# Kernel tuning notes

Measured on AMD Instinct MI355X. Metric: run time of the kernel, lower is better.

## Reference

```python
import jax, jax.numpy as jnp
import numpy as np

B, C, H, W = 32, 256, 64, 64
N_HEAD, LDIM = 4, 64
HW = H * W
SCALE = float(np.sqrt(LDIM))
EPS = 1e-5


def setup_inputs() -> dict:
    key = jax.random.key(0)
    ks = jax.random.split(key, 8)
    inp = {
        "x": jax.random.normal(ks[0], (B, C, H, W), dtype=jnp.float32),
        "x1": jax.random.normal(ks[1], (B, C, H, W), dtype=jnp.float32),
        # linear weights stored as [in, out] (transposed torch layout)
        "Wq": jax.random.normal(ks[2], (HW, N_HEAD * LDIM), dtype=jnp.float32) * 0.02,
        "Wk": jax.random.normal(ks[3], (HW, N_HEAD * LDIM), dtype=jnp.float32) * 0.02,
        "Wv": jax.random.normal(ks[4], (HW, N_HEAD * LDIM), dtype=jnp.float32) * 0.02,
        "Wfc": jax.random.normal(ks[5], (N_HEAD * LDIM, HW), dtype=jnp.float32) * 0.02,
        "gamma": jnp.ones((C,), dtype=jnp.float32),
        "beta": jnp.zeros((C,), dtype=jnp.float32),
    }
    return inp


def reference(x, x1, Wq, Wk, Wv, Wfc, gamma, beta):
    b, c, h, w = x.shape
    xf = x.reshape(b, c, h * w)    # [b, c, hw]
    x1f = x1.reshape(b, c, h * w)
    # projections: [b, c, hw] @ [hw, n*d] -> [b, c, n*d]
    q = (xf @ Wq).reshape(b, c, N_HEAD, LDIM).transpose(0, 2, 1, 3)   # [b, n, c, d]
    k = (x1f @ Wk).reshape(b, c, N_HEAD, LDIM).transpose(0, 2, 1, 3)
    v = (x1f @ Wv).reshape(b, c, N_HEAD, LDIM).transpose(0, 2, 1, 3)
    # scaled dot-product attention over the c 'channel-token' axis
    attn = jnp.einsum('bncd,bnmd->bncm', q / SCALE, k)  # [b, n, c, c]
    attn = jax.nn.softmax(attn, axis=-1)
    out = jnp.einsum('bncm,bnmd->bncd', attn, v)        # [b, n, c, d]
    out = out.transpose(0, 2, 1, 3).reshape(b, c, N_HEAD * LDIM)
    out = (out @ Wfc).reshape(b, c, h, w)
    # BatchNorm2d (training-mode batch statistics, biased variance)
    mean = out.mean(axis=(0, 2, 3), keepdims=True)
    var = out.var(axis=(0, 2, 3), keepdims=True)
    out = (out - mean) * jax.lax.rsqrt(var + EPS)
    out = out * gamma[None, :, None, None] + beta[None, :, None, None]
    return out
```

## Files before the change

### kernel.cpp

```cpp
#include <hip/hip_runtime.h>
#include <hip/hip_bf16.h>

#define Bsz 32
#define Csz 256
#define HWsz 4096
#define NDsz 256
#define Msz 8192

typedef __bf16 bf16x8 __attribute__((ext_vector_type(8)));
typedef float  f32x4  __attribute__((ext_vector_type(4)));
typedef short  s16x4  __attribute__((ext_vector_type(4)));
typedef short  s16x8  __attribute__((ext_vector_type(8)));

__device__ __forceinline__ unsigned short f2bf(float f){
  unsigned u = __float_as_uint(f);
  u += 0x7FFFu + ((u >> 16) & 1u);
  return (unsigned short)(u >> 16);
}

__device__ __forceinline__ f32x4 mfma16(bf16x8 a, bf16x8 b, f32x4 c){
  return __builtin_amdgcn_mfma_f32_16x16x32_bf16(a, b, c, 0, 0, 0);
}

__global__ void k_prep(const float* __restrict__ Wq, const float* __restrict__ Wk,
                       const float* __restrict__ Wv, const float* __restrict__ Wfc,
                       unsigned short* __restrict__ Wt, unsigned short* __restrict__ Wfct){
  __shared__ float t[32][33];
  int z = blockIdx.z;
  int bx = blockIdx.x, by = blockIdx.y;
  const float* src; unsigned short* dst; int R, Ct;
  if (z < 3) {
    src = (z == 0) ? Wq : (z == 1 ? Wk : Wv);
    dst = Wt + (size_t)z * Csz * HWsz;  R = HWsz; Ct = NDsz;
  } else {
    int tidx = bx * 8 + by; bx = tidx & 7; by = tidx >> 3;
    src = Wfc; dst = Wfct; R = NDsz; Ct = HWsz;
  }
  int tx = threadIdx.x, ty = threadIdx.y;
  int i0 = bx * 32, j0 = by * 32;
  #pragma unroll
  for (int r = 0; r < 4; r++)
    t[ty + 8*r][tx] = src[(size_t)(i0 + ty + 8*r) * Ct + j0 + tx];
  __syncthreads();
  #pragma unroll
  for (int r = 0; r < 4; r++)
    dst[(size_t)(j0 + ty + 8*r) * R + i0 + tx] = f2bf(t[tx][ty + 8*r]);
}

__global__ __launch_bounds__(256, 3) void k_proj(const float* __restrict__ X,
    const float* __restrict__ X1, const unsigned short* __restrict__ Wt,
    unsigned short* __restrict__ QKV){
  const int wgid = blockIdx.x;
  const int xcd = wgid & 7, q = wgid >> 3;
  const int rtHi = q / 6, m = q - rtHi * 6;
  const int rt = rtHi * 8 + xcd;
  const int which = m >> 1, ct = m & 1;

  const float* A = (which == 0) ? X : X1;
  const unsigned short* Bt = Wt + (size_t)which * NDsz * HWsz;
  unsigned short* Cp = QKV + (size_t)which * Msz * NDsz;

  __shared__ unsigned short As[64][72];
  __shared__ unsigned short Bs[128][72];

  const int tid = threadIdx.x;
  const int lane = tid & 63, w = tid >> 6;
  const int l15 = lane & 15, l4 = lane >> 4;
  const int wm = w >> 1, wn = w & 1;

  const int arow = tid >> 2, acol = (tid & 3) * 16;
  const float* agp = A + (size_t)(rt*64 + arow) * HWsz + acol;
  const int brow = tid >> 1, bcol = (tid & 1) * 32;
  const unsigned short* bgp = Bt + (size_t)(ct*128 + brow) * HWsz + bcol;

  f32x4 acc[2][4] = {};
  float4 ar[4];
  s16x8 br[4];

#define LOADA(kt) { _Pragma("unroll") for (int i = 0; i < 4; i++) \
    ar[i] = *(const float4*)(agp + (size_t)(kt)*64 + i*4); }
#define LOADB(kt) { _Pragma("unroll") for (int p = 0; p < 4; p++) \
    br[p] = *(const s16x8*)(bgp + (size_t)(kt)*64 + p*8); }
#define WRITEAB { _Pragma("unroll") for (int i = 0; i < 4; i++){ s16x4 cv; \
      cv[0]=(short)f2bf(ar[i].x); cv[1]=(short)f2bf(ar[i].y); \
      cv[2]=(short)f2bf(ar[i].z); cv[3]=(short)f2bf(ar[i].w); \
      *(s16x4*)&As[arow][acol + i*4] = cv; } \
    _Pragma("unroll") for (int p = 0; p < 4; p++) *(s16x8*)&Bs[brow][bcol + p*8] = br[p]; }

  LOADA(0); LOADB(0);
  WRITEAB;
  __syncthreads();

  const int NK = HWsz / 64;
  for (int kt = 1; kt <= NK; kt++){
    const bool more = (kt < NK);
    if (more){ LOADA(kt); LOADB(kt); }
    #pragma unroll
    for (int kk = 0; kk < 2; kk++){
      bf16x8 a[2], b[4];
      #pragma unroll
      for (int fm = 0; fm < 2; fm++) a[fm] = *(const bf16x8*)&As[wm*32 + fm*16 + l15][kk*32 + l4*8];
      #pragma unroll
      for (int fn = 0; fn < 4; fn++) b[fn] = *(const bf16x8*)&Bs[wn*64 + fn*16 + l15][kk*32 + l4*8];
      #pragma unroll
      for (int fm = 0; fm < 2; fm++)
        #pragma unroll
        for (int fn = 0; fn < 4; fn++)
          acc[fm][fn] = mfma16(a[fm], b[fn], acc[fm][fn]);
    }
    if (more){
      __syncthreads();
      WRITEAB;
      __syncthreads();
    }
  }
#undef LOADA
#undef LOADB
#undef WRITEAB
  #pragma unroll
  for (int fm = 0; fm < 2; fm++)
    #pragma unroll
    for (int fn = 0; fn < 4; fn++)
      #pragma unroll
      for (int r = 0; r < 4; r++)
        Cp[(size_t)(rt*64 + wm*32 + fm*16 + l4*4 + r) * NDsz
           + ct*128 + wn*64 + fn*16 + l15] = f2bf(acc[fm][fn][r]);
}

__global__ __launch_bounds__(256) void k_attn(const unsigned short* __restrict__ Q,
    const unsigned short* __restrict__ K, const unsigned short* __restrict__ V,
    unsigned short* __restrict__ O){
  const int b = blockIdx.x >> 3, n = (blockIdx.x >> 1) & 3, half = blockIdx.x & 1;
  __shared__ unsigned short VT[64][264];
  __shared__ unsigned short PL[4][32][72];

  const int tid = threadIdx.x;
  const int lane = tid & 63, w = tid >> 6;
  const int l15 = lane & 15, l4 = lane >> 4;

  {
    const unsigned short* vp = V + (size_t)(b*256 + tid) * NDsz + n*64;
    #pragma unroll
    for (int j = 0; j < 8; j++){
      s16x8 vv = *(const s16x8*)(vp + j*8);
      #pragma unroll
      for (int e = 0; e < 8; e++) VT[j*8 + e][tid] = (unsigned short)vv[e];
    }
  }

  const int qbase = b*256 + half*128 + w*32;
  bf16x8 qf[2][2];
  #pragma unroll
  for (int fm = 0; fm < 2; fm++)
    #pragma unroll
    for (int ks = 0; ks < 2; ks++)
      qf[fm][ks] = *(const bf16x8*)(Q + (size_t)(qbase + fm*16 + l15) * NDsz
                                      + n*64 + ks*32 + l4*8);

  f32x4 oacc[2][4] = {};
  float rs[2][4] = {};
  __syncthreads();

  for (int ch = 0; ch < 4; ch++){
    f32x4 sacc[2][4] = {};
    #pragma unroll
    for (int ks = 0; ks < 2; ks++){
      bf16x8 kf[4];
      #pragma unroll
      for (int fn = 0; fn < 4; fn++)
        kf[fn] = *(const bf16x8*)(K + (size_t)(b*256 + ch*64 + fn*16 + l15) * NDsz
                                    + n*64 + ks*32 + l4*8);
      #pragma unroll
      for (int fm = 0; fm < 2; fm++)
        #pragma unroll
        for (int fn = 0; fn < 4; fn++)
          sacc[fm][fn] = mfma16(qf[fm][ks], kf[fn], sacc[fm][fn]);
    }
    #pragma unroll
    for (int fm = 0; fm < 2; fm++)
      #pragma unroll
      for (int fn = 0; fn < 4; fn++)
        #pragma unroll
        for (int r = 0; r < 4; r++){
          float e = __expf(sacc[fm][fn][r] * 0.125f);
          rs[fm][r] += e;
          PL[w][fm*16 + l4*4 + r][fn*16 + l15] = f2bf(e);
        }
    #pragma unroll
    for (int ks = 0; ks < 2; ks++){
      bf16x8 pa[2], vb[4];
      #pragma unroll
      for (int fm = 0; fm < 2; fm++)
        pa[fm] = *(const bf16x8*)&PL[w][fm*16 + l15][ks*32 + l4*8];
      #pragma unroll
      for (int fn = 0; fn < 4; fn++)
        vb[fn] = *(const bf16x8*)&VT[fn*16 + l15][ch*64 + ks*32 + l4*8];
      #pragma unroll
      for (int fm = 0; fm < 2; fm++)
        #pragma unroll
        for (int fn = 0; fn < 4; fn++)
          oacc[fm][fn] = mfma16(pa[fm], vb[fn], oacc[fm][fn]);
    }
  }
  #pragma unroll
  for (int fm = 0; fm < 2; fm++)
    #pragma unroll
    for (int r = 0; r < 4; r++){
      float s = rs[fm][r];
      s += __shfl_xor(s, 1, 16); s += __shfl_xor(s, 2, 16);
      s += __shfl_xor(s, 4, 16); s += __shfl_xor(s, 8, 16);
      rs[fm][r] = 1.0f / s;
    }
  #pragma unroll
  for (int fm = 0; fm < 2; fm++)
    #pragma unroll
    for (int fn = 0; fn < 4; fn++)
      #pragma unroll
      for (int r = 0; r < 4; r++)
        O[(size_t)(qbase + fm*16 + l4*4 + r) * NDsz + n*64 + fn*16 + l15] =
            f2bf(oacc[fm][fn][r] * rs[fm][r]);
}

__global__ __launch_bounds__(256) void k_fc(const unsigned short* __restrict__ AO,
    const unsigned short* __restrict__ Wfct, float* __restrict__ Y,
    float* __restrict__ rowsum, float* __restrict__ rowsq){
  const int ct = blockIdx.x, rt = blockIdx.y;
  __shared__ union UU {
    struct { unsigned short As[64][72]; unsigned short Bs[256][72]; } st;
    float Cs[4][64][68];
  } u;
  __shared__ float sRow[4][64], sRowQ[4][64];
  const int tid = threadIdx.x;
  const int lane = tid & 63, w = tid >> 6;
  const int l15 = lane & 15, l4 = lane >> 4;

  const int arow = tid >> 2, acol = (tid & 3) * 16;
  const unsigned short* agp = AO + (size_t)(rt*64 + arow) * NDsz + acol;
  const int brow = tid >> 3, bcol = (tid & 7) * 8;
  const unsigned short* bgp = Wfct + (size_t)(ct*256 + brow) * NDsz + bcol;

  f32x4 acc[4][4] = {};
  s16x8 ar2[2];
  s16x8 br[8];

#define LOADA(kt) { _Pragma("unroll") for (int i = 0; i < 2; i++) \
    ar2[i] = *(const s16x8*)(agp + (kt)*64 + i*8); }
#define LOADB(kt) { _Pragma("unroll") for (int p = 0; p < 8; p++) \
    br[p] = *(const s16x8*)(bgp + (size_t)p*32*NDsz + (kt)*64); }
#define WRITEAB { _Pragma("unroll") for (int i = 0; i < 2; i++) \
    *(s16x8*)&u.st.As[arow][acol + i*8] = ar2[i]; \
    _Pragma("unroll") for (int p = 0; p < 8; p++) *(s16x8*)&u.st.Bs[p*32 + brow][bcol] = br[p]; }

  LOADA(0); LOADB(0);
  WRITEAB;
  __syncthreads();

  const int NK = NDsz / 64;
  for (int kt = 1; kt <= NK; kt++){
    const bool more = (kt < NK);
    if (more){ LOADA(kt); LOADB(kt); }
    #pragma unroll
    for (int kk = 0; kk < 2; kk++){
      bf16x8 a[4], b[4];
      #pragma unroll
      for (int fm = 0; fm < 4; fm++) a[fm] = *(const bf16x8*)&u.st.As[fm*16 + l15][kk*32 + l4*8];
      #pragma unroll
      for (int fn = 0; fn < 4; fn++) b[fn] = *(const bf16x8*)&u.st.Bs[w*64 + fn*16 + l15][kk*32 + l4*8];
      #pragma unroll
      for (int fm = 0; fm < 4; fm++)
        #pragma unroll
        for (int fn = 0; fn < 4; fn++)
          acc[fm][fn] = mfma16(a[fm], b[fn], acc[fm][fn]);
    }
    if (more){
      __syncthreads();
      WRITEAB;
      __syncthreads();
    }
  }
#undef LOADA
#undef LOADB
#undef WRITEAB
  float prs[4][4], prq[4][4];
  #pragma unroll
  for (int fm = 0; fm < 4; fm++)
    #pragma unroll
    for (int r = 0; r < 4; r++){
      float s = 0.f, qq = 0.f;
      #pragma unroll
      for (int fn = 0; fn < 4; fn++){ float v = acc[fm][fn][r]; s += v; qq += v*v; }
      s  += __shfl_xor(s, 1, 16);  s += __shfl_xor(s, 2, 16);
      s  += __shfl_xor(s, 4, 16);  s += __shfl_xor(s, 8, 16);
      qq += __shfl_xor(qq, 1, 16); qq += __shfl_xor(qq, 2, 16);
      qq += __shfl_xor(qq, 4, 16); qq += __shfl_xor(qq, 8, 16);
      prs[fm][r] = s; prq[fm][r] = qq;
    }
  __syncthreads();
  if (l15 == 0){
    #pragma unroll
    for (int fm = 0; fm < 4; fm++)
      #pragma unroll
      for (int r = 0; r < 4; r++){
        int row = fm*16 + l4*4 + r;
        sRow[w][row]  = prs[fm][r];
        sRowQ[w][row] = prq[fm][r];
      }
  }
  #pragma unroll
  for (int fm = 0; fm < 4; fm++)
    #pragma unroll
    for (int fn = 0; fn < 4; fn++)
      #pragma unroll
      for (int r = 0; r < 4; r++)
        u.Cs[w][fm*16 + l4*4 + r][fn*16 + l15] = acc[fm][fn][r];
  __syncthreads();
  if (tid < 64){
    float s = sRow[0][tid] + sRow[1][tid] + sRow[2][tid] + sRow[3][tid];
    float qq = sRowQ[0][tid] + sRowQ[1][tid] + sRowQ[2][tid] + sRowQ[3][tid];
    atomicAdd(&rowsum[rt*64 + tid], s);
    atomicAdd(&rowsq[rt*64 + tid], qq);
  }
  #pragma unroll
  for (int i = 0; i < 16; i++){
    int linear = i*64 + lane;
    int row = linear >> 4, f4 = linear & 15;
    float4 v = *(const float4*)&u.Cs[w][row][f4*4];
    *(float4*)(Y + (size_t)(rt*64 + row) * HWsz + ct*256 + w*64 + f4*4) = v;
  }
}

__global__ __launch_bounds__(256) void k_bnred(const float* __restrict__ rowsum,
    const float* __restrict__ rowsq, const float* __restrict__ gamma,
    const float* __restrict__ beta, float* __restrict__ scale,
    float* __restrict__ shift){
  const int t = threadIdx.x;
  const int c = blockIdx.x * 32 + (t & 31);
  const int part = t >> 5;
  float s = 0.f, qq = 0.f;
  #pragma unroll
  for (int j = 0; j < 4; j++){
    int row = (part*4 + j) * 256 + c;
    s += rowsum[row]; qq += rowsq[row];
  }
  __shared__ float ls[8][32], lq[8][32];
  ls[part][t & 31] = s; lq[part][t & 31] = qq;
  __syncthreads();
  if (t < 32){
    float S = 0.f, Q = 0.f;
    #pragma unroll
    for (int p = 0; p < 8; p++){ S += ls[p][t]; Q += lq[p][t]; }
    const float inv = 1.0f / (float)(Bsz * HWsz);
    float mean = S * inv;
    float var  = Q * inv - mean*mean;
    float istd = rsqrtf(var + 1e-5f);
    float g = gamma[c] * istd;
    scale[c] = g;
    shift[c] = beta[c] - mean * g;
  }
}

__global__ __launch_bounds__(256) void k_apply(float* __restrict__ Y,
    const float* __restrict__ scale, const float* __restrict__ shift){
  const int NF4 = Msz * HWsz / 4;
  int gstride = gridDim.x * blockDim.x;
  for (int F = blockIdx.x * blockDim.x + threadIdx.x; F < NF4; F += gstride){
    int c = (F >> 10) & 255;
    float4 v = ((const float4*)Y)[F];
    float sc = scale[c], sh = shift[c];
    v.x = v.x*sc + sh; v.y = v.y*sc + sh; v.z = v.z*sc + sh; v.w = v.w*sc + sh;
    ((float4*)Y)[F] = v;
  }
}

extern "C" void kernel_launch(void* const* d_in, const int* in_sizes, int n_in,
                              void* d_out, int out_size, void* d_ws, size_t ws_size,
                              hipStream_t stream){
  const float* x     = (const float*)d_in[0];
  const float* x1    = (const float*)d_in[1];
  const float* Wq    = (const float*)d_in[2];
  const float* Wk    = (const float*)d_in[3];
  const float* Wv    = (const float*)d_in[4];
  const float* Wfc   = (const float*)d_in[5];
  const float* gamma = (const float*)d_in[6];
  const float* beta  = (const float*)d_in[7];
  float* Y = (float*)d_out;

  unsigned short* Wt   = (unsigned short*)d_ws;
  unsigned short* Wfct = Wt + (size_t)3*Csz*HWsz;
  unsigned short* QKV  = Wfct + (size_t)HWsz*NDsz;
  unsigned short* AO   = QKV + (size_t)3*Msz*NDsz;
  float* rowsum = (float*)(AO + (size_t)Msz*NDsz);
  float* rowsq  = rowsum + Msz;
  float* scale  = rowsq + Msz;
  float* shift  = scale + 256;

  hipMemsetAsync(rowsum, 0, 2 * Msz * sizeof(float), stream);

  k_prep <<<dim3(128, 8, 4), dim3(32, 8), 0, stream>>>(Wq, Wk, Wv, Wfc, Wt, Wfct);
  k_proj <<<dim3(768),       dim3(256),   0, stream>>>(x, x1, Wt, QKV);
  k_attn <<<dim3(256),       dim3(256),   0, stream>>>(QKV, QKV + (size_t)Msz*NDsz,
                                                       QKV + (size_t)2*Msz*NDsz, AO);
  k_fc   <<<dim3(16, 128),   dim3(256),   0, stream>>>(AO, Wfct, Y, rowsum, rowsq);
  k_bnred<<<dim3(8),         dim3(256),   0, stream>>>(rowsum, rowsq, gamma, beta, scale, shift);
  k_apply<<<dim3(2048),      dim3(256),   0, stream>>>(Y, scale, shift);
}
```

Before: 549.3 us.

## Restructure projection GEMM: 32-row tiles, full-N per block, fused K/V sharing A

The projection kernel now uses 32-row M tiles that cover all 256 output columns. Each of 512 blocks converts its fp32 activation tile to bf16 once and stores it in LDS, and K and V blocks share that tile across two weight matrices. Weight fragments are read directly from global memory into registers instead of being staged through LDS. The change removes redundant fp32 activation reads and conversions (previously repeated for each column tile and for K and V). In exchange it relies on cache bandwidth for uncoalesced per-lane weight loads and produces uneven work between Q blocks and K/V blocks.

```diff
diff --git a/kernel.cpp b/kernel.cpp
--- a/kernel.cpp
+++ b/kernel.cpp
@@ -47,84 +47,93 @@
     dst[(size_t)(j0 + ty + 8*r) * R + i0 + tx] = f2bf(t[tx][ty + 8*r]);
 }
 
-__global__ __launch_bounds__(256, 3) void k_proj(const float* __restrict__ X,
+__global__ __launch_bounds__(256) void k_proj(const float* __restrict__ X,
     const float* __restrict__ X1, const unsigned short* __restrict__ Wt,
     unsigned short* __restrict__ QKV){
-  const int wgid = blockIdx.x;
-  const int xcd = wgid & 7, q = wgid >> 3;
-  const int rtHi = q / 6, m = q - rtHi * 6;
-  const int rt = rtHi * 8 + xcd;
-  const int which = m >> 1, ct = m & 1;
-
-  const float* A = (which == 0) ? X : X1;
-  const unsigned short* Bt = Wt + (size_t)which * NDsz * HWsz;
-  unsigned short* Cp = QKV + (size_t)which * Msz * NDsz;
-
-  __shared__ unsigned short As[64][72];
-  __shared__ unsigned short Bs[128][72];
-
-  const int tid = threadIdx.x;
-  const int lane = tid & 63, w = tid >> 6;
+  const int bid = blockIdx.x;
+  const bool iskv = bid >= 256;
+  const int rt = iskv ? bid - 256 : bid;
+  const float* A = iskv ? X1 : X;
+  const unsigned short* B0 = Wt + (iskv ? (size_t)NDsz * HWsz : 0);
+  const unsigned short* B1 = Wt + (size_t)2 * NDsz * HWsz;
+  unsigned short* O0 = QKV + (iskv ? (size_t)Msz * NDsz : 0);
+  unsigned short* O1 = QKV + (size_t)2 * Msz * NDsz;
+
+  __shared__ unsigned short As[32][136];
+
+  const int tid = threadIdx.x, lane = tid & 63, w = tid >> 6;
   const int l15 = lane & 15, l4 = lane >> 4;
-  const int wm = w >> 1, wn = w & 1;
-
-  const int arow = tid >> 2, acol = (tid & 3) * 16;
-  const float* agp = A + (size_t)(rt*64 + arow) * HWsz + acol;
-  const int brow = tid >> 1, bcol = (tid & 1) * 32;
-  const unsigned short* bgp = Bt + (size_t)(ct*128 + brow) * HWsz + bcol;
-
-  f32x4 acc[2][4] = {};
+  const int arow = tid >> 3, acol = (tid & 7) * 16;
+  const float* agp = A + (size_t)(rt*32 + arow) * HWsz + acol;
+
+  const unsigned short* bp0[4];
+  const unsigned short* bp1[4];
+  #pragma unroll
+  for (int fn = 0; fn < 4; fn++){
+    bp0[fn] = B0 + (size_t)(w*64 + fn*16 + l15) * HWsz;
+    bp1[fn] = B1 + (size_t)(w*64 + fn*16 + l15) * HWsz;
+  }
+
+  f32x4 acc0[2][4] = {};
+  f32x4 acc1[2][4] = {};
   float4 ar[4];
-  s16x8 br[4];
 
 #define LOADA(kt) { _Pragma("unroll") for (int i = 0; i < 4; i++) \
-    ar[i] = *(const float4*)(agp + (size_t)(kt)*64 + i*4); }
-#define LOADB(kt) { _Pragma("unroll") for (int p = 0; p < 4; p++) \
-    br[p] = *(const s16x8*)(bgp + (size_t)(kt)*64 + p*8); }
-#define WRITEAB { _Pragma("unroll") for (int i = 0; i < 4; i++){ s16x4 cv; \
-      cv[0]=(short)f2bf(ar[i].x); cv[1]=(short)f2bf(ar[i].y); \
-      cv[2]=(short)f2bf(ar[i].z); cv[3]=(short)f2bf(ar[i].w); \
-      *(s16x4*)&As[arow][acol + i*4] = cv; } \
-    _Pragma("unroll") for (int p = 0; p < 4; p++) *(s16x8*)&Bs[brow][bcol + p*8] = br[p]; }
-
-  LOADA(0); LOADB(0);
-  WRITEAB;
-  __syncthreads();
-
-  const int NK = HWsz / 64;
-  for (int kt = 1; kt <= NK; kt++){
-    const bool more = (kt < NK);
-    if (more){ LOADA(kt); LOADB(kt); }
-    #pragma unroll
-    for (int kk = 0; kk < 2; kk++){
-      bf16x8 a[2], b[4];
-      #pragma unroll
-      for (int fm = 0; fm < 2; fm++) a[fm] = *(const bf16x8*)&As[wm*32 + fm*16 + l15][kk*32 + l4*8];
-      #pragma unroll
-      for (int fn = 0; fn < 4; fn++) b[fn] = *(const bf16x8*)&Bs[wn*64 + fn*16 + l15][kk*32 + l4*8];
-      #pragma unroll
-      for (int fm = 0; fm < 2; fm++)
+    ar[i] = *(const float4*)(agp + (size_t)(kt)*128 + i*4); }
+#define WRITEA { _Pragma("unroll") for (int i = 0; i < 2; i++){ s16x8 cv; \
+      _Pragma("unroll") for (int j = 0; j < 2; j++){ float4 f = ar[i*2+j]; \
+        cv[j*4+0]=(short)f2bf(f.x); cv[j*4+1]=(short)f2bf(f.y); \
+        cv[j*4+2]=(short)f2bf(f.z); cv[j*4+3]=(short)f2bf(f.w); } \
+      *(s16x8*)&As[arow][acol + i*8] = cv; } }
+
+  LOADA(0);
+  WRITEA;
+  __syncthreads();
+
+  const int NK = HWsz / 128;
+  for (int kt = 0; kt < NK; kt++){
+    const bool more = (kt + 1 < NK);
+    if (more) LOADA(kt + 1);
+    const size_t kb = (size_t)kt * 128;
+    #pragma unroll
+    for (int kk = 0; kk < 4; kk++){
+      const size_t kcol = kb + kk*32 + l4*8;
+      bf16x8 a0 = *(const bf16x8*)&As[     l15][kk*32 + l4*8];
+      bf16x8 a1 = *(const bf16x8*)&As[16 + l15][kk*32 + l4*8];
+      #pragma unroll
+      for (int fn = 0; fn < 4; fn++){
+        bf16x8 b = *(const bf16x8*)(bp0[fn] + kcol);
+        acc0[0][fn] = mfma16(a0, b, acc0[0][fn]);
+        acc0[1][fn] = mfma16(a1, b, acc0[1][fn]);
+      }
+      if (iskv){
         #pragma unroll
-        for (int fn = 0; fn < 4; fn++)
-          acc[fm][fn] = mfma16(a[fm], b[fn], acc[fm][fn]);
-    }
+        for (int fn = 0; fn < 4; fn++){
+          bf16x8 b = *(const bf16x8*)(bp1[fn] + kcol);
+          acc1[0][fn] = mfma16(a0, b, acc1[0][fn]);
+          acc1[1][fn] = mfma16(a1, b, acc1[1][fn]);
+        }
+      }
+    }
+    __syncthreads();
     if (more){
+      WRITEA;
       __syncthreads();
-      WRITEAB;
-      __syncthreads();
     }
   }
 #undef LOADA
-#undef LOADB
-#undef WRITEAB
+#undef WRITEA
   #pragma unroll
   for (int fm = 0; fm < 2; fm++)
     #pragma unroll
     for (int fn = 0; fn < 4; fn++)
       #pragma unroll
-      for (int r = 0; r < 4; r++)
-        Cp[(size_t)(rt*64 + wm*32 + fm*16 + l4*4 + r) * NDsz
-           + ct*128 + wn*64 + fn*16 + l15] = f2bf(acc[fm][fn][r]);
+      for (int r = 0; r < 4; r++){
+        const size_t row = rt*32 + fm*16 + l4*4 + r;
+        O0[row * NDsz + w*64 + fn*16 + l15] = f2bf(acc0[fm][fn][r]);
+        if (iskv)
+          O1[row * NDsz + w*64 + fn*16 + l15] = f2bf(acc1[fm][fn][r]);
+      }
 }
 
 __global__ __launch_bounds__(256) void k_attn(const unsigned short* __restrict__ Q,
@@ -397,7 +406,7 @@
   hipMemsetAsync(rowsum, 0, 2 * Msz * sizeof(float), stream);
 
   k_prep <<<dim3(128, 8, 4), dim3(32, 8), 0, stream>>>(Wq, Wk, Wv, Wfc, Wt, Wfct);
-  k_proj <<<dim3(768),       dim3(256),   0, stream>>>(x, x1, Wt, QKV);
+  k_proj <<<dim3(512),       dim3(256),   0, stream>>>(x, x1, Wt, QKV);
   k_attn <<<dim3(256),       dim3(256),   0, stream>>>(QKV, QKV + (size_t)Msz*NDsz,
                                                        QKV + (size_t)2*Msz*NDsz, AO);
   k_fc   <<<dim3(16, 128),   dim3(256),   0, stream>>>(AO, Wfct, Y, rowsum, rowsq);
```

After: 622.4 us. +13.3%, slower.
